# Kernel optimization log

Measured on AMD Instinct MI355X. Metric: run time of the kernel, lower is better.

The kernel has to match this reference:

```python
import jax, jax.numpy as jnp
import numpy as np

SIGMA = 0.07        # kernel width param; gamma = 1/sigma
K_NEG = 16          # hard negatives per anchor
BS = 8192
DIM = 256

def setup_inputs() -> dict:
    key = jax.random.key(0)
    features = jax.random.normal(key, (BS, 2, DIM), dtype=jnp.float32)
    return {"features": features}

def reference(features):
    gamma = 1.0 / float(SIGMA)
    F1 = features[:, 0, :].astype(jnp.float32)   # (bs, d)
    F2 = features[:, 1, :].astype(jnp.float32)   # (bs, d)
    # RBF-style kernel: exp(-gamma * (2 - 2 * F1 @ F2^T))
    K = jnp.exp(-gamma * (2.0 - 2.0 * jnp.einsum('id,jd->ij', F1, F2)))  # (bs, bs)
    pos_loss = jnp.mean(jnp.diagonal(K))
    # mask diagonal with -inf, take row-wise top-k, mean over all selected
    eye = jnp.eye(BS, dtype=bool)
    neg = jnp.where(eye, -jnp.inf, K)
    topk_vals, _ = jax.lax.top_k(neg, K_NEG)     # (bs, k)
    hard_neg_loss = jnp.mean(topk_vals)
    return (-pos_loss, hard_neg_loss)
```

## Files before the change

### kernel.cpp

```cpp
#include <hip/hip_runtime.h>
#include <math.h>

#define BS   8192
#define DIM  256
#define KNEG 16
#define GAMMA (1.0f / 0.07f)
#define EXP_CLAMP 60.0f
#define NSTRIPS 8

typedef float v4f  __attribute__((ext_vector_type(4)));
typedef short s8b  __attribute__((ext_vector_type(8)));

__device__ __forceinline__ float sat_exp(float dot) {
    float a = 2.0f * GAMMA * dot - 2.0f * GAMMA;
    return expf(fminf(a, EXP_CLAMP));
}

__device__ __forceinline__ void ce(float& x, float& y) {
    float lo = fminf(x, y), hi = fmaxf(x, y);
    x = lo; y = hi;
}

__device__ __forceinline__ void sort16(float (&a)[16]) {
    ce(a[0],a[1]); ce(a[2],a[3]); ce(a[4],a[5]); ce(a[6],a[7]);
    ce(a[8],a[9]); ce(a[10],a[11]); ce(a[12],a[13]); ce(a[14],a[15]);
    ce(a[0],a[2]); ce(a[1],a[3]); ce(a[4],a[6]); ce(a[5],a[7]);
    ce(a[8],a[10]); ce(a[9],a[11]); ce(a[12],a[14]); ce(a[13],a[15]);
    ce(a[1],a[2]); ce(a[5],a[6]); ce(a[9],a[10]); ce(a[13],a[14]);
    ce(a[0],a[4]); ce(a[1],a[5]); ce(a[2],a[6]); ce(a[3],a[7]);
    ce(a[8],a[12]); ce(a[9],a[13]); ce(a[10],a[14]); ce(a[11],a[15]);
    ce(a[2],a[4]); ce(a[3],a[5]); ce(a[10],a[12]); ce(a[11],a[13]);
    ce(a[1],a[2]); ce(a[3],a[4]); ce(a[5],a[6]);
    ce(a[9],a[10]); ce(a[11],a[12]); ce(a[13],a[14]);
    ce(a[0],a[8]); ce(a[1],a[9]); ce(a[2],a[10]); ce(a[3],a[11]);
    ce(a[4],a[12]); ce(a[5],a[13]); ce(a[6],a[14]); ce(a[7],a[15]);
    ce(a[4],a[8]); ce(a[5],a[9]); ce(a[6],a[10]); ce(a[7],a[11]);
    ce(a[2],a[4]); ce(a[3],a[5]); ce(a[6],a[8]); ce(a[7],a[9]);
    ce(a[10],a[12]); ce(a[11],a[13]);
    ce(a[1],a[2]); ce(a[3],a[4]); ce(a[5],a[6]); ce(a[7],a[8]);
    ce(a[9],a[10]); ce(a[11],a[12]); ce(a[13],a[14]);
}

__device__ __forceinline__ void merge_top16(float (&lst)[16], const float (&nw)[16]) {
#pragma unroll
    for (int i = 0; i < 16; ++i) lst[i] = fmaxf(lst[i], nw[15 - i]);
#pragma unroll
    for (int j = 8; j > 0; j >>= 1)
#pragma unroll
        for (int i = 0; i < 16; ++i) {
            int ixj = i ^ j;
            if (ixj > i) ce(lst[i], lst[ixj]);
        }
}

__device__ __forceinline__ void topk_insert(float (&lst)[16], float v) {
    float nl[16];
#pragma unroll
    for (int u = 0; u < 15; ++u)
        nl[u] = (v > lst[u + 1]) ? lst[u + 1] : ((v > lst[u]) ? v : lst[u]);
    nl[15] = (v > lst[15]) ? v : lst[15];
#pragma unroll
    for (int u = 0; u < 16; ++u) lst[u] = nl[u];
}

__device__ __forceinline__ unsigned short f2bf_rne(float f) {
    unsigned int u = __float_as_uint(f);
    u += 0x7FFFu + ((u >> 16) & 1u);
    return (unsigned short)(u >> 16);
}

__device__ __forceinline__ void gld_lds16(const void* g, void* l) {
    __builtin_amdgcn_global_load_lds(
        (const __attribute__((address_space(1))) void*)g,
        (__attribute__((address_space(3))) void*)l, 16, 0, 0);
}

__device__ __forceinline__ float finite_or(float x, float repl) {
    if (isnan(x)) return repl;
    if (isinf(x)) return x > 0.0f ? 3.0e38f : -3.0e38f;
    return x;
}

__global__ void conv_pos(const float* __restrict__ feat,
                         unsigned short* __restrict__ featbf,
                         float* __restrict__ partialPos,
                         unsigned int* __restrict__ ticket) {
    __shared__ float red[8];
    if (blockIdx.x == 0 && threadIdx.x == 0) *ticket = 0u;
    int t = blockIdx.x * 256 + threadIdx.x;
    int row = t >> 5;
    int c = t & 31;
    const float* f1 = feat + (size_t)row * 512 + c * 8;
    const float* f2 = f1 + 256;
    float4 a0 = *(const float4*)(f1);
    float4 a1 = *(const float4*)(f1 + 4);
    float4 b0 = *(const float4*)(f2);
    float4 b1 = *(const float4*)(f2 + 4);
    uint4 pa, pb;
    pa.x = (unsigned)f2bf_rne(a0.x) | ((unsigned)f2bf_rne(a0.y) << 16);
    pa.y = (unsigned)f2bf_rne(a0.z) | ((unsigned)f2bf_rne(a0.w) << 16);
    pa.z = (unsigned)f2bf_rne(a1.x) | ((unsigned)f2bf_rne(a1.y) << 16);
    pa.w = (unsigned)f2bf_rne(a1.z) | ((unsigned)f2bf_rne(a1.w) << 16);
    pb.x = (unsigned)f2bf_rne(b0.x) | ((unsigned)f2bf_rne(b0.y) << 16);
    pb.y = (unsigned)f2bf_rne(b0.z) | ((unsigned)f2bf_rne(b0.w) << 16);
    pb.z = (unsigned)f2bf_rne(b1.x) | ((unsigned)f2bf_rne(b1.y) << 16);
    pb.w = (unsigned)f2bf_rne(b1.z) | ((unsigned)f2bf_rne(b1.w) << 16);
    *(uint4*)(featbf + (size_t)row * 512 + c * 8) = pa;
    *(uint4*)(featbf + (size_t)row * 512 + 256 + c * 8) = pb;
    float p = a0.x * b0.x + a0.y * b0.y + a0.z * b0.z + a0.w * b0.w
            + a1.x * b1.x + a1.y * b1.y + a1.z * b1.z + a1.w * b1.w;
#pragma unroll
    for (int o = 16; o; o >>= 1) p += __shfl_xor(p, o, 32);
    if (c == 0) red[threadIdx.x >> 5] = sat_exp(p);
    __syncthreads();
    if (threadIdx.x == 0) {
        float s = 0.0f;
#pragma unroll
        for (int i = 0; i < 8; ++i) s += red[i];
        partialPos[blockIdx.x] = s;
    }
}

#define A_OFF  32768
#define S1_LDS 49152

__global__ __launch_bounds__(256, 3) void stage1(const unsigned short* __restrict__ featbf,
                                                 float* __restrict__ wsTop) {
    __shared__ __align__(16) char smem[S1_LDS];
    const int t = threadIdx.x;
    const int l = t & 63;
    const int w = t >> 6;
    const int wy = w >> 1, wx = w & 1;
    const int quad = l >> 4, lane16 = l & 15;
    const int nbase = blockIdx.x * 64;
    const int strip = blockIdx.y;

#pragma unroll
    for (int jj = 0; jj < 8; ++jj) {
        int j = w * 8 + jj;
        int r = 2 * j + (l >> 5);
        int c = (l & 31) ^ (r & 31);
        gld_lds16(featbf + ((size_t)(nbase + r) << 9) + c * 8, smem + j * 1024);
    }

    float lst[2][16];
#pragma unroll
    for (int ni = 0; ni < 2; ++ni)
#pragma unroll
        for (int i = 0; i < 16; ++i) lst[ni][i] = -INFINITY;

    const int akey = (quad ^ ((lane16 >> 1) & 3)) * 16;
    int ab[2];
#pragma unroll
    for (int jj = 0; jj < 2; ++jj) {
        int r = 16 * (w * 2 + jj) + (l >> 2);
        int c = (l & 3) ^ ((r >> 1) & 3);
        ab[jj] = (r << 9) + c * 8;
    }

    {
        const int u0 = (strip * 1024 << 9) + 256;
#pragma unroll
        for (int jj = 0; jj < 2; ++jj)
            gld_lds16(featbf + (size_t)(u0 + ab[jj]),
                      smem + A_OFF + (w * 2 + jj) * 1024);
    }

#pragma unroll 1
    for (int ct = 0; ct < 8; ++ct) {
        const int ctbase = strip * 1024 + ct * 128;
        v4f acc[4][2];
#pragma unroll
        for (int mi = 0; mi < 4; ++mi)
#pragma unroll
            for (int ni = 0; ni < 2; ++ni) acc[mi][ni] = (v4f)0.0f;

#pragma unroll
        for (int s = 0; s < 8; ++s) {
            __syncthreads();
            if (ct < 7 || s < 7) {
                const int nct = (s == 7) ? ctbase + 128 : ctbase;
                const int ns = (s == 7) ? 0 : s + 1;
                const int u = (nct << 9) + 256 + ns * 32;
                char* dst = smem + A_OFF + ((s + 1) & 1) * 8192 + w * 2048;
#pragma unroll
                for (int jj = 0; jj < 2; ++jj)
                    gld_lds16(featbf + (size_t)(u + ab[jj]), dst + jj * 1024);
            }
            const char* Ab = smem + A_OFF + (s & 1) * 8192;
            s8b a[4];
#pragma unroll
            for (int mi = 0; mi < 4; ++mi)
                a[mi] = *(const s8b*)(Ab + (wx * 64 + mi * 16 + lane16) * 64 + akey);
#pragma unroll
            for (int ni = 0; ni < 2; ++ni) {
                int n31 = ni * 16 + lane16;
                s8b b = *(const s8b*)(smem
                    + (wy * 32 + n31) * 512 + (((s * 4 + quad) ^ n31) & 31) * 16);
#pragma unroll
                for (int mi = 0; mi < 4; ++mi)
                    acc[mi][ni] = __builtin_amdgcn_mfma_f32_16x16x32_bf16(
                        a[mi], b, acc[mi][ni], 0, 0, 0);
            }
        }
#pragma unroll
        for (int ni = 0; ni < 2; ++ni) {
            const int row = nbase + wy * 32 + ni * 16 + lane16;
            float nw[16];
#pragma unroll
            for (int mi = 0; mi < 4; ++mi) {
                const int c0 = ctbase + wx * 64 + mi * 16 + quad * 4;
#pragma unroll
                for (int r4 = 0; r4 < 4; ++r4) {
                    float v = acc[mi][ni][r4];
                    nw[mi * 4 + r4] = (c0 + r4 == row) ? -INFINITY : v;
                }
            }
            sort16(nw);
            merge_top16(lst[ni], nw);
        }
    }
#pragma unroll
    for (int ni = 0; ni < 2; ++ni) {
#pragma unroll
        for (int r = 16; r <= 32; r <<= 1) {
            float nw[16];
#pragma unroll
            for (int i = 0; i < 16; ++i) nw[i] = __shfl(lst[ni][i], l ^ r, 64);
            merge_top16(lst[ni], nw);
        }
    }
    __syncthreads();
    float* mrg = (float*)(smem + A_OFF);
    if (wx == 1 && quad == 0) {
#pragma unroll
        for (int ni = 0; ni < 2; ++ni) {
            int rl = wy * 32 + ni * 16 + lane16;
#pragma unroll
            for (int i = 0; i < 16; i += 4)
                *(v4f*)(mrg + rl * 16 + i) = *(v4f*)&lst[ni][i];
        }
    }
    __syncthreads();
    if (wx == 0 && quad == 0) {
#pragma unroll
        for (int ni = 0; ni < 2; ++ni) {
            const int rl = wy * 32 + ni * 16 + lane16;
            float nw[16];
#pragma unroll
            for (int i = 0; i < 16; ++i) nw[i] = mrg[rl * 16 + i];
            merge_top16(lst[ni], nw);
            float* dst = wsTop + ((size_t)(nbase + rl) * NSTRIPS + strip) * 16;
#pragma unroll
            for (int i = 0; i < 16; i += 4)
                *(float4*)(dst + i) = make_float4(lst[ni][i], lst[ni][i + 1],
                                                  lst[ni][i + 2], lst[ni][i + 3]);
        }
    }
}

__global__ void stage2_fused(const float* __restrict__ wsTop,
                             const float* __restrict__ partialPos,
                             float* __restrict__ partialNeg,
                             unsigned int* __restrict__ ticket,
                             float* __restrict__ out) {
    __shared__ float red[128];
    __shared__ int isLast;
    int tid = blockIdx.x * 128 + threadIdx.x;
    int row = tid >> 1, half = tid & 1;
    const float* src = wsTop + (size_t)row * (NSTRIPS * 16) + half * 64;
    float lst[16];
#pragma unroll
    for (int i = 0; i < 16; ++i) lst[i] = src[i];
#pragma unroll
    for (int c = 16; c < 64; c += 16) {
        float nw[16];
#pragma unroll
        for (int i = 0; i < 16; ++i) nw[i] = src[c + i];
        merge_top16(lst, nw);
    }
    {
        float nw[16];
        int pl = (threadIdx.x & 63) ^ 1;
#pragma unroll
        for (int i = 0; i < 16; ++i) nw[i] = __shfl(lst[i], pl, 64);
        merge_top16(lst, nw);
    }
    float s = 0.0f;
#pragma unroll
    for (int i = 0; i < 16; ++i) s += sat_exp(lst[i]);
    red[threadIdx.x] = half ? 0.0f : s;
    __syncthreads();
    for (int o = 64; o; o >>= 1) {
        if (threadIdx.x < o) red[threadIdx.x] += red[threadIdx.x + o];
        __syncthreads();
    }
    if (threadIdx.x == 0) partialNeg[blockIdx.x] = red[0];
    __threadfence();
    if (threadIdx.x == 0) isLast = (atomicAdd(ticket, 1u) == 127u) ? 1 : 0;
    __syncthreads();
    if (isLast) {
        float sp = 0.0f, sn = 0.0f;
        for (int i = threadIdx.x; i < 1024; i += 128) sp += partialPos[i];
        sn = partialNeg[threadIdx.x];
#pragma unroll
        for (int o = 32; o; o >>= 1) {
            sp += __shfl_xor(sp, o, 64);
            sn += __shfl_xor(sn, o, 64);
        }
        __syncthreads();
        if ((threadIdx.x & 63) == 0) {
            red[(threadIdx.x >> 6)] = sp;
            red[2 + (threadIdx.x >> 6)] = sn;
        }
        __syncthreads();
        if (threadIdx.x == 0) {
            float tp = red[0] + red[1];
            float tn = red[2] + red[3];
            out[0] = finite_or(-(tp / (float)BS), 0.0f);
            out[1] = finite_or(tn / (float)(BS * KNEG), 0.0f);
        }
    }
}

__global__ void init_acc(float* acc) {
    if (threadIdx.x < 64) acc[threadIdx.x] = 0.0f;
}

__global__ void pos_kernel(const float* __restrict__ feat, float* __restrict__ acc) {
    int t = blockIdx.x * 256 + threadIdx.x;
    int row = t >> 4;
    int lane16 = t & 15;
    const float* f = feat + (size_t)row * 512 + lane16 * 16;
    float p = 0.0f;
#pragma unroll
    for (int q = 0; q < 16; q += 4) {
        float4 a = *(const float4*)(f + q);
        float4 b = *(const float4*)(f + 256 + q);
        p += a.x * b.x + a.y * b.y + a.z * b.z + a.w * b.w;
    }
#pragma unroll
    for (int o = 8; o; o >>= 1) p += __shfl_xor(p, o, 16);
    if (lane16 == 0) atomicAdd(&acc[0], sat_exp(p));
}

#define L_AOFF   0
#define L_BOFF   10240
#define L_PITCH  80
#define CPITCH  272
#define CWAVE   17408
#define L_SMEM  69632
__global__ __launch_bounds__(256, 2) void stage1_legacy(const float* __restrict__ feat,
                                                        float* __restrict__ wsTop) {
    __shared__ __align__(16) char smem[L_SMEM];
    const int t = threadIdx.x;
    const int l = t & 63;
    const int w = t >> 6;
    const int wy = w >> 1, wx = w & 1;
    const int quad = l >> 4, lane16 = l & 15;
    const int rowbase = blockIdx.x * 128;
    const int strip = blockIdx.y;
    char* cw = smem + w * CWAVE;
    const int grow = rowbase + wy * 64 + l;

    float lst[16];
#pragma unroll
    for (int i = 0; i < 16; ++i) lst[i] = -INFINITY;

    for (int ct = 0; ct < 4; ++ct) {
        const int colbase = strip * 1024 + ct * 256;
        v4f acc[4][8];
#pragma unroll
        for (int mi = 0; mi < 4; ++mi)
#pragma unroll
            for (int ni = 0; ni < 8; ++ni) acc[mi][ni] = (v4f)0.0f;
        for (int s = 0; s < 8; ++s) {
            const int k0 = s * 32;
            __syncthreads();
#pragma unroll
            for (int i = 0; i < 4; ++i) {
                int c = i * 256 + t;
                int r = c >> 3, chk = c & 7;
                float4 v = *(const float4*)(feat + (size_t)(rowbase + r) * 512 + k0 + chk * 4);
                uint2 pk;
                pk.x = (unsigned)f2bf_rne(v.x) | ((unsigned)f2bf_rne(v.y) << 16);
                pk.y = (unsigned)f2bf_rne(v.z) | ((unsigned)f2bf_rne(v.w) << 16);
                *(uint2*)(smem + L_AOFF + r * L_PITCH + chk * 8) = pk;
            }
#pragma unroll
            for (int i = 0; i < 8; ++i) {
                int c = i * 256 + t;
                int n = c >> 3, chk = c & 7;
                float4 v = *(const float4*)(feat + (size_t)(colbase + n) * 512 + 256 + k0 + chk * 4);
                uint2 pk;
                pk.x = (unsigned)f2bf_rne(v.x) | ((unsigned)f2bf_rne(v.y) << 16);
                pk.y = (unsigned)f2bf_rne(v.z) | ((unsigned)f2bf_rne(v.w) << 16);
                *(uint2*)(smem + L_BOFF + n * L_PITCH + chk * 8) = pk;
            }
            __syncthreads();
            s8b a[4];
#pragma unroll
            for (int mi = 0; mi < 4; ++mi)
                a[mi] = *(const s8b*)(smem + L_AOFF + (wy * 64 + mi * 16 + lane16) * L_PITCH + quad * 16);
#pragma unroll
            for (int ni = 0; ni < 8; ++ni) {
                s8b b = *(const s8b*)(smem + L_BOFF + (wx * 128 + ni * 16 + lane16) * L_PITCH + quad * 16);
#pragma unroll
                for (int mi = 0; mi < 4; ++mi)
                    acc[mi][ni] = __builtin_amdgcn_mfma_f32_16x16x32_bf16(a[mi], b, acc[mi][ni], 0, 0, 0);
            }
        }
#pragma unroll
        for (int h = 0; h < 2; ++h) {
            __syncthreads();
#pragma unroll
            for (int ni = 0; ni < 4; ++ni) {
                int c = ni * 16 + lane16;
#pragma unroll
                for (int mi = 0; mi < 4; ++mi)
                    *(v4f*)(cw + c * CPITCH + mi * 64 + quad * 16) = acc[mi][h * 4 + ni];
            }
            __syncthreads();
            const int gc0 = colbase + wx * 128 + h * 64;
            const int dj = grow - gc0;
#pragma unroll
            for (int j = 0; j < 64; ++j) {
                float v = *(const float*)(cw + j * CPITCH + l * 4);
                if (v > lst[0] && j != dj) topk_insert(lst, v);
            }
        }
    }
    float* dst = wsTop + (size_t)grow * 256 + strip * 32 + wx * 16;
#pragma unroll
    for (int i = 0; i < 16; i += 4)
        *(float4*)(dst + i) = make_float4(lst[i], lst[i + 1], lst[i + 2], lst[i + 3]);
}

__global__ void stage2_legacy(const float* __restrict__ wsTop, float* __restrict__ acc) {
    int row = blockIdx.x * blockDim.x + threadIdx.x;
    if (row >= BS) return;
    const float* src = wsTop + (size_t)row * 256;
    float lst[16];
#pragma unroll
    for (int i = 0; i < 16; ++i) lst[i] = -INFINITY;
    for (int c = 0; c < 256; c += 4) {
        float4 v4 = *(const float4*)(src + c);
        float vv[4] = {v4.x, v4.y, v4.z, v4.w};
#pragma unroll
        for (int j = 0; j < 4; ++j)
            if (vv[j] > lst[0]) topk_insert(lst, vv[j]);
    }
    float s = 0.0f;
#pragma unroll
    for (int i = 0; i < 16; ++i) s += sat_exp(lst[i]);
    atomicAdd(&acc[1], s);
}

__global__ void final_legacy(const float* __restrict__ acc, float* __restrict__ out) {
    if (threadIdx.x == 0) {
        out[0] = finite_or(-(acc[0] / (float)BS), 0.0f);
        out[1] = finite_or(acc[1] / (float)(BS * KNEG), 0.0f);
    }
}

extern "C" void kernel_launch(void* const* d_in, const int* in_sizes, int n_in,
                              void* d_out, int out_size, void* d_ws, size_t ws_size,
                              hipStream_t stream) {
    const float* feat = (const float*)d_in[0];
    float* out = (float*)d_out;

    unsigned short* featbf = (unsigned short*)d_ws;
    float* wsTop = (float*)(featbf + (size_t)BS * 512);
    float* partialPos = wsTop + (size_t)BS * NSTRIPS * 16;
    float* partialNeg = partialPos + 1024;
    unsigned int* ticket = (unsigned int*)(partialNeg + 128);
    const size_t need_new = (size_t)BS * 512 * 2 + (size_t)BS * NSTRIPS * 16 * 4
                          + (1024 + 128 + 1) * 4;

    if (ws_size >= need_new) {
        conv_pos<<<1024, 256, 0, stream>>>(feat, featbf, partialPos, ticket);
        stage1<<<dim3(128, NSTRIPS), 256, 0, stream>>>(featbf, wsTop);
        stage2_fused<<<128, 128, 0, stream>>>(wsTop, partialPos, partialNeg, ticket, out);
    } else {
        float* acc = (float*)d_ws;
        float* wsTopL = acc + 64;
        init_acc<<<1, 64, 0, stream>>>(acc);
        pos_kernel<<<512, 256, 0, stream>>>(feat, acc);
        stage1_legacy<<<dim3(64, 8), 256, 0, stream>>>(feat, wsTopL);
        stage2_legacy<<<32, 256, 0, stream>>>(wsTopL, acc);
        final_legacy<<<1, 1, 0, stream>>>(acc, out);
    }
}
```

Measured before the change: 138.8 us.

## Stream B operand per k-step instead of keeping whole row tile resident in LDS

Until now the 64-row anchor tile (full 256-dim bf16) stayed resident in 32 KB of LDS for the whole strip. Now it is reloaded in 32-column slices alongside the A slices in a double buffer, which halves LDS per block so launch bounds can go from 3 to 4 waves per SIMD. This trades repeated global/L2 reads of the anchor rows (reloaded for each of 8 column tiles) for higher occupancy and latency hiding.

```diff
diff --git a/kernel.cpp b/kernel.cpp
--- a/kernel.cpp
+++ b/kernel.cpp
@@ -121,10 +121,10 @@
     }
 }
 
-#define A_OFF  32768
-#define S1_LDS 49152
-
-__global__ __launch_bounds__(256, 3) void stage1(const unsigned short* __restrict__ featbf,
+#define BUFSZ  12288
+#define S1_LDS 24576
+
+__global__ __launch_bounds__(256, 4) void stage1(const unsigned short* __restrict__ featbf,
                                                  float* __restrict__ wsTop) {
     __shared__ __align__(16) char smem[S1_LDS];
     const int t = threadIdx.x;
@@ -135,14 +135,6 @@
     const int nbase = blockIdx.x * 64;
     const int strip = blockIdx.y;
 
-#pragma unroll
-    for (int jj = 0; jj < 8; ++jj) {
-        int j = w * 8 + jj;
-        int r = 2 * j + (l >> 5);
-        int c = (l & 31) ^ (r & 31);
-        gld_lds16(featbf + ((size_t)(nbase + r) << 9) + c * 8, smem + j * 1024);
-    }
-
     float lst[2][16];
 #pragma unroll
     for (int ni = 0; ni < 2; ++ni)
@@ -153,17 +145,24 @@
     int ab[2];
 #pragma unroll
     for (int jj = 0; jj < 2; ++jj) {
-        int r = 16 * (w * 2 + jj) + (l >> 2);
-        int c = (l & 3) ^ ((r >> 1) & 3);
-        ab[jj] = (r << 9) + c * 8;
-    }
-
+        int ra = 16 * (w * 2 + jj) + (l >> 2);
+        int ca = (l & 3) ^ ((ra >> 1) & 3);
+        ab[jj] = (ra << 9) + ca * 8;
+    }
+    int bb;
     {
-        const int u0 = (strip * 1024 << 9) + 256;
+        int rb = 16 * w + (l >> 2);
+        int cb = (l & 3) ^ (rb & 3);
+        bb = (rb << 9) + cb * 8;
+    }
+    const int ubase = nbase << 9;
+
+    {
+        const int uA = (strip * 1024 << 9) + 256;
 #pragma unroll
         for (int jj = 0; jj < 2; ++jj)
-            gld_lds16(featbf + (size_t)(u0 + ab[jj]),
-                      smem + A_OFF + (w * 2 + jj) * 1024);
+            gld_lds16(featbf + (size_t)(uA + ab[jj]), smem + (w * 2 + jj) * 1024);
+        gld_lds16(featbf + (size_t)(ubase + bb), smem + 8192 + w * 1024);
     }
 
 #pragma unroll 1
@@ -181,22 +180,24 @@
             if (ct < 7 || s < 7) {
                 const int nct = (s == 7) ? ctbase + 128 : ctbase;
                 const int ns = (s == 7) ? 0 : s + 1;
-                const int u = (nct << 9) + 256 + ns * 32;
-                char* dst = smem + A_OFF + ((s + 1) & 1) * 8192 + w * 2048;
+                const int uA = (nct << 9) + 256 + ns * 32;
+                const int uB = ubase + ns * 32;
+                char* dst = smem + ((s + 1) & 1) * BUFSZ;
 #pragma unroll
                 for (int jj = 0; jj < 2; ++jj)
-                    gld_lds16(featbf + (size_t)(u + ab[jj]), dst + jj * 1024);
-            }
-            const char* Ab = smem + A_OFF + (s & 1) * 8192;
+                    gld_lds16(featbf + (size_t)(uA + ab[jj]),
+                              dst + (w * 2 + jj) * 1024);
+                gld_lds16(featbf + (size_t)(uB + bb), dst + 8192 + w * 1024);
+            }
+            const char* Ab = smem + (s & 1) * BUFSZ;
             s8b a[4];
 #pragma unroll
             for (int mi = 0; mi < 4; ++mi)
                 a[mi] = *(const s8b*)(Ab + (wx * 64 + mi * 16 + lane16) * 64 + akey);
 #pragma unroll
             for (int ni = 0; ni < 2; ++ni) {
-                int n31 = ni * 16 + lane16;
-                s8b b = *(const s8b*)(smem
-                    + (wy * 32 + n31) * 512 + (((s * 4 + quad) ^ n31) & 31) * 16);
+                int rl = wy * 32 + ni * 16 + lane16;
+                s8b b = *(const s8b*)(Ab + 8192 + rl * 64 + ((quad ^ (rl & 3)) * 16));
 #pragma unroll
                 for (int mi = 0; mi < 4; ++mi)
                     acc[mi][ni] = __builtin_amdgcn_mfma_f32_16x16x32_bf16(
@@ -231,7 +232,7 @@
         }
     }
     __syncthreads();
-    float* mrg = (float*)(smem + A_OFF);
+    float* mrg = (float*)smem;
     if (wx == 1 && quad == 0) {
 #pragma unroll
         for (int ni = 0; ni < 2; ++ni) {
```

After: 143.7 us. 1.03x slower.
